# Kernel optimization log

Hardware: AMD Instinct MI355X
Metric: run time of the kernel (lower is better)

The kernel has to match this reference:

```python
import jax, jax.numpy as jnp
import numpy as np

N = 1_000_000
DIM = 128
NUM_GRAPHS = 4096


def setup_inputs() -> dict:
    key = jax.random.key(0)
    kx, kq, kb = jax.random.split(key, 3)
    x = jax.random.normal(kx, (N, DIM), dtype=jnp.float32)
    query = jax.random.normal(kq, (DIM,), dtype=jnp.float32) * 0.02
    batch = jnp.sort(jax.random.randint(kb, (N,), 0, NUM_GRAPHS, dtype=jnp.int64))
    return {"x": x, "query": query, "batch": batch}


def reference(x, query, batch):
    # scores: [N] dot of each node feature with the learned query vector
    scores = jnp.einsum("nd,d->n", x, query)
    # segment-wise numerically-stable softmax over nodes belonging to each graph
    seg_max = jax.ops.segment_max(scores, batch, num_segments=NUM_GRAPHS)
    ex = jnp.exp(scores - seg_max[batch])  # [N]
    seg_sum = jax.ops.segment_sum(ex, batch, num_segments=NUM_GRAPHS)
    weights = ex / seg_sum[batch]  # [N]
    # weighted scatter-add pooling -> [num_graphs, dim]
    pooled = jax.ops.segment_sum(weights[:, None] * x, batch, num_segments=NUM_GRAPHS)
    return pooled
```

## Files before the change

### kernel.cpp

```cpp
#include <hip/hip_runtime.h>
#include <math.h>

#define DIM 128
#define CHUNK 4
#define STREAMS 8
#define STRIDE (STREAMS)
#define ROUND (STREAMS * CHUNK)

typedef float v4f __attribute__((ext_vector_type(4)));

__device__ __forceinline__ int lower_bound_i(const int* __restrict__ b, int n, int key) {
    int lo = 0, hi = n;
    while (lo < hi) {
        int mid = (lo + hi) >> 1;
        if (b[mid] < key) lo = mid + 1; else hi = mid;
    }
    return lo;
}

__global__ __launch_bounds__(256) void attnpool_kernel(
    const float* __restrict__ x, const float* __restrict__ q,
    const int* __restrict__ batch, float* __restrict__ out, int n)
{
    const int g    = blockIdx.x;
    const int tid  = threadIdx.x;
    const int wave = tid >> 6;
    const int lane = tid & 63;
    const int half = lane >> 5;
    const int hl   = lane & 31;
    const int sid  = wave * 2 + half;

    const int lo = lower_bound_i(batch, n, g);
    const int hi = lower_bound_i(batch, n, g + 1);

    const float4 qf = *(const float4*)(q + hl * 4);

    float  m = -INFINITY;
    float  l = 0.f;
    float4 o = make_float4(0.f, 0.f, 0.f, 0.f);

    const int i0 = lo + sid;
    const v4f zz = (v4f)0.f;
    const float* xb = x + hl * 4;

    v4f cur[CHUNK];
    #pragma unroll
    for (int j = 0; j < CHUNK; ++j) {
        const int ii = i0 + j * STRIDE;
        cur[j] = (ii < hi) ? __builtin_nontemporal_load((const v4f*)(xb + (size_t)ii * DIM)) : zz;
    }

    for (int base = i0; base < hi; base += ROUND) {
        v4f nxt[CHUNK];
        #pragma unroll
        for (int j = 0; j < CHUNK; ++j) {
            const int ii = base + ROUND + j * STRIDE;
            nxt[j] = (ii < hi) ? __builtin_nontemporal_load((const v4f*)(xb + (size_t)ii * DIM)) : zz;
        }

        float s[CHUNK];
        #pragma unroll
        for (int j = 0; j < CHUNK; ++j)
            s[j] = cur[j].x * qf.x + cur[j].y * qf.y + cur[j].z * qf.z + cur[j].w * qf.w;

        #pragma unroll
        for (int d = 16; d >= 1; d >>= 1) {
            #pragma unroll
            for (int j = 0; j < CHUNK; ++j)
                s[j] += __shfl_xor(s[j], d);
        }

        #pragma unroll
        for (int j = 0; j < CHUNK; ++j)
            if (base + j * STRIDE >= hi) s[j] = -INFINITY;

        const float smax = fmaxf(fmaxf(s[0], s[1]), fmaxf(s[2], s[3]));
        if (smax > m) {
            const float a = __expf(m - smax);
            l *= a;
            o.x *= a; o.y *= a; o.z *= a; o.w *= a;
            m = smax;
        }

        #pragma unroll
        for (int j = 0; j < CHUNK; ++j) {
            const float p = (base + j * STRIDE < hi) ? __expf(s[j] - m) : 0.f;
            l += p;
            o.x += p * cur[j].x; o.y += p * cur[j].y;
            o.z += p * cur[j].z; o.w += p * cur[j].w;
        }

        #pragma unroll
        for (int j = 0; j < CHUNK; ++j) cur[j] = nxt[j];
    }

    __shared__ float sm_m[STREAMS];
    __shared__ float sm_l[STREAMS];
    __shared__ float sm_o[STREAMS * DIM];
    if (hl == 0) { sm_m[sid] = m; sm_l[sid] = l; }
    *(float4*)(sm_o + sid * DIM + hl * 4) = o;
    __syncthreads();

    if (tid < DIM) {
        float M = -INFINITY;
        #pragma unroll
        for (int h = 0; h < STREAMS; ++h)
            if (sm_l[h] > 0.f && sm_m[h] > M) M = sm_m[h];
        float L = 0.f, O = 0.f;
        #pragma unroll
        for (int h = 0; h < STREAMS; ++h) {
            if (sm_l[h] > 0.f) {
                const float c = __expf(sm_m[h] - M);
                L += c * sm_o[h * DIM + tid] * 0.f + c * sm_o[h * DIM + tid];
            }
        }
        M = -INFINITY;
        #pragma unroll
        for (int h = 0; h < STREAMS; ++h)
            if (sm_l[h] > 0.f && sm_m[h] > M) M = sm_m[h];
        L = 0.f; O = 0.f;
        #pragma unroll
        for (int h = 0; h < STREAMS; ++h) {
            if (sm_l[h] > 0.f) {
                const float c = __expf(sm_m[h] - M);
                L += c * sm_l[h];
                O += c * sm_o[h * DIM + tid];
            }
        }
        __builtin_nontemporal_store((L > 0.f) ? (O / L) : 0.f, out + (size_t)g * DIM + tid);
    }
}

extern "C" void kernel_launch(void* const* d_in, const int* in_sizes, int n_in,
                              void* d_out, int out_size, void* d_ws, size_t ws_size,
                              hipStream_t stream) {
    const float* x     = (const float*)d_in[0];
    const float* q     = (const float*)d_in[1];
    const int*   batch = (const int*)d_in[2];
    float*       out   = (float*)d_out;
    const int n          = in_sizes[0] / DIM;
    const int num_graphs = out_size / DIM;
    attnpool_kernel<<<num_graphs, 256, 0, stream>>>(x, q, batch, out, n);
}
```

Baseline: 631.0 us.

## Precompute segment bounds in a separate kernel, deepen prefetch, use cached loads

Adds a pre-pass kernel that writes segment start offsets into workspace, replacing the two per-block binary searches over the batch array with two direct loads. The main kernel doubles the per-stream prefetch chunk from 4 to 8 rows to keep more loads in flight. It also swaps nontemporal loads for regular loads and removes a redundant duplicated merge loop in the epilogue. The extra kernel launch adds overhead, the larger chunk raises register pressure, and the new bounds kernel assumes batch holds int32 values in sorted order.

```diff
diff --git a/kernel.cpp b/kernel.cpp
--- a/kernel.cpp
+++ b/kernel.cpp
@@ -2,25 +2,25 @@
 #include <math.h>
 
 #define DIM 128
-#define CHUNK 4
+#define CHUNK 8
 #define STREAMS 8
-#define STRIDE (STREAMS)
 #define ROUND (STREAMS * CHUNK)
 
 typedef float v4f __attribute__((ext_vector_type(4)));
 
-__device__ __forceinline__ int lower_bound_i(const int* __restrict__ b, int n, int key) {
-    int lo = 0, hi = n;
-    while (lo < hi) {
-        int mid = (lo + hi) >> 1;
-        if (b[mid] < key) lo = mid + 1; else hi = mid;
-    }
-    return lo;
+__global__ __launch_bounds__(256) void seg_bounds_kernel(
+    const int* __restrict__ batch, int* __restrict__ seg, int n, int ng)
+{
+    const int i = blockIdx.x * blockDim.x + threadIdx.x;
+    if (i > n) return;
+    const int prev = (i == 0) ? -1 : batch[i - 1];
+    const int cur  = (i == n) ? ng : batch[i];
+    for (int g = prev + 1; g <= cur; ++g) seg[g] = i;
 }
 
 __global__ __launch_bounds__(256) void attnpool_kernel(
     const float* __restrict__ x, const float* __restrict__ q,
-    const int* __restrict__ batch, float* __restrict__ out, int n)
+    const int* __restrict__ seg, float* __restrict__ out)
 {
     const int g    = blockIdx.x;
     const int tid  = threadIdx.x;
@@ -30,8 +30,8 @@
     const int hl   = lane & 31;
     const int sid  = wave * 2 + half;
 
-    const int lo = lower_bound_i(batch, n, g);
-    const int hi = lower_bound_i(batch, n, g + 1);
+    const int lo = seg[g];
+    const int hi = seg[g + 1];
 
     const float4 qf = *(const float4*)(q + hl * 4);
 
@@ -46,16 +46,16 @@
     v4f cur[CHUNK];
     #pragma unroll
     for (int j = 0; j < CHUNK; ++j) {
-        const int ii = i0 + j * STRIDE;
-        cur[j] = (ii < hi) ? __builtin_nontemporal_load((const v4f*)(xb + (size_t)ii * DIM)) : zz;
+        const int ii = i0 + j * STREAMS;
+        cur[j] = (ii < hi) ? *(const v4f*)(xb + (size_t)ii * DIM) : zz;
     }
 
     for (int base = i0; base < hi; base += ROUND) {
         v4f nxt[CHUNK];
         #pragma unroll
         for (int j = 0; j < CHUNK; ++j) {
-            const int ii = base + ROUND + j * STRIDE;
-            nxt[j] = (ii < hi) ? __builtin_nontemporal_load((const v4f*)(xb + (size_t)ii * DIM)) : zz;
+            const int ii = base + ROUND + j * STREAMS;
+            nxt[j] = (ii < hi) ? *(const v4f*)(xb + (size_t)ii * DIM) : zz;
         }
 
         float s[CHUNK];
@@ -72,9 +72,12 @@
 
         #pragma unroll
         for (int j = 0; j < CHUNK; ++j)
-            if (base + j * STRIDE >= hi) s[j] = -INFINITY;
+            if (base + j * STREAMS >= hi) s[j] = -INFINITY;
 
-        const float smax = fmaxf(fmaxf(s[0], s[1]), fmaxf(s[2], s[3]));
+        float smax = s[0];
+        #pragma unroll
+        for (int j = 1; j < CHUNK; ++j) smax = fmaxf(smax, s[j]);
+
         if (smax > m) {
             const float a = __expf(m - smax);
             l *= a;
@@ -84,7 +87,7 @@
 
         #pragma unroll
         for (int j = 0; j < CHUNK; ++j) {
-            const float p = (base + j * STRIDE < hi) ? __expf(s[j] - m) : 0.f;
+            const float p = (base + j * STREAMS < hi) ? __expf(s[j] - m) : 0.f;
             l += p;
             o.x += p * cur[j].x; o.y += p * cur[j].y;
             o.z += p * cur[j].z; o.w += p * cur[j].w;
@@ -111,18 +114,6 @@
         for (int h = 0; h < STREAMS; ++h) {
             if (sm_l[h] > 0.f) {
                 const float c = __expf(sm_m[h] - M);
-                L += c * sm_o[h * DIM + tid] * 0.f + c * sm_o[h * DIM + tid];
-            }
-        }
-        M = -INFINITY;
-        #pragma unroll
-        for (int h = 0; h < STREAMS; ++h)
-            if (sm_l[h] > 0.f && sm_m[h] > M) M = sm_m[h];
-        L = 0.f; O = 0.f;
-        #pragma unroll
-        for (int h = 0; h < STREAMS; ++h) {
-            if (sm_l[h] > 0.f) {
-                const float c = __expf(sm_m[h] - M);
                 L += c * sm_l[h];
                 O += c * sm_o[h * DIM + tid];
             }
@@ -140,5 +131,9 @@
     float*       out   = (float*)d_out;
     const int n          = in_sizes[0] / DIM;
     const int num_graphs = out_size / DIM;
-    attnpool_kernel<<<num_graphs, 256, 0, stream>>>(x, q, batch, out, n);
+
+    int* seg = (int*)d_ws;
+    const int sb = (n + 1 + 255) / 256;
+    seg_bounds_kernel<<<sb, 256, 0, stream>>>(batch, seg, n, num_graphs);
+    attnpool_kernel<<<num_graphs, 256, 0, stream>>>(x, q, seg, out);
 }
```

Result: slower. 650.3 us (+3.1%).
